# Performance work log

Measured on AMD Instinct MI355X. Metric: run time of the kernel, lower is better.

Reference implementation:

```python
import jax, jax.numpy as jnp
import numpy as np

B, S, H = 2, 2048, 2048
NH, NKV, HD = 16, 4, 128
GROUPS = NH // NKV  # 4
ROPE_BASE = 10000.0


def _rope_tables(seq_len, dim):
    inv_freq = 1.0 / (ROPE_BASE ** (jnp.arange(0, dim, 2, dtype=jnp.float32) / dim))
    t = jnp.arange(seq_len, dtype=jnp.float32)
    freqs = jnp.outer(t, inv_freq)            # [S, HD/2]
    emb = jnp.concatenate([freqs, freqs], -1)  # [S, HD]
    return jnp.cos(emb), jnp.sin(emb)


def _rotate_half(x):
    x1, x2 = x[..., : x.shape[-1] // 2], x[..., x.shape[-1] // 2:]
    return jnp.concatenate([-x2, x1], axis=-1)


def setup_inputs() -> dict:
    key = jax.random.key(0)
    ks = jax.random.split(key, 5)
    hidden_states = jax.random.normal(ks[0], (B, S, H), dtype=jnp.float32)
    wq = jax.random.normal(ks[1], (H, NH * HD), dtype=jnp.float32) * 0.02
    wk = jax.random.normal(ks[2], (H, NKV * HD), dtype=jnp.float32) * 0.02
    wv = jax.random.normal(ks[3], (H, NKV * HD), dtype=jnp.float32) * 0.02
    wo = jax.random.normal(ks[4], (NH * HD, H), dtype=jnp.float32) * 0.02
    # additive causal mask [1,1,S,S]
    causal = jnp.tril(jnp.ones((S, S), dtype=bool))
    attention_mask = jnp.where(causal, 0.0, jnp.finfo(jnp.float32).min)[None, None]
    return {"hidden_states": hidden_states, "attention_mask": attention_mask,
            "wq": wq, "wk": wk, "wv": wv, "wo": wo}


def reference(hidden_states, attention_mask, wq, wk, wv, wo):
    b, s, _ = hidden_states.shape
    # projections -> [B, heads, S, HD]
    q = (hidden_states @ wq).reshape(b, s, NH, HD).transpose(0, 2, 1, 3)
    k = (hidden_states @ wk).reshape(b, s, NKV, HD).transpose(0, 2, 1, 3)
    v = (hidden_states @ wv).reshape(b, s, NKV, HD).transpose(0, 2, 1, 3)
    cos, sin = _rope_tables(s, HD)             # [S, HD]
    cos = cos[None, None]; sin = sin[None, None]
    q = q * cos + _rotate_half(q) * sin
    k = k * cos + _rotate_half(k) * sin
    # GQA: repeat kv heads (matches repeat_interleave on dim=1)
    k = jnp.repeat(k, GROUPS, axis=1)
    v = jnp.repeat(v, GROUPS, axis=1)
    scores = jnp.einsum("bhqd,bhkd->bhqk", q, k) / jnp.sqrt(jnp.float32(HD))
    scores = scores + attention_mask
    probs = jax.nn.softmax(scores.astype(jnp.float32), axis=-1).astype(q.dtype)
    attn = jnp.einsum("bhqk,bhkd->bhqd", probs, v)
    attn = attn.transpose(0, 2, 1, 3).reshape(b, s, NH * HD)
    return attn @ wo
```

## Files before the change

### kernel.cpp

```cpp
#include <hip/hip_runtime.h>

typedef unsigned short u16;
typedef unsigned int u32;
typedef __attribute__((ext_vector_type(8))) __bf16 bf16x8;
typedef __attribute__((ext_vector_type(8))) u16 u16x8;
typedef __attribute__((ext_vector_type(4))) float f32x4;

#define B_ 2
#define S_ 2048
#define H_ 2048
#define NH_ 16
#define NKV_ 4
#define HD_ 128

__device__ __forceinline__ u16 f2bf(float f) {
  return __builtin_bit_cast(u16, static_cast<__bf16>(f));
}
__device__ __forceinline__ float bf2f(u16 v) {
  return __builtin_bit_cast(float, (u32)v << 16);
}
__device__ __forceinline__ void gl2lds16(const void* g, void* l) {
  __builtin_amdgcn_global_load_lds((const __attribute__((address_space(1))) u32*)g,
                                   (__attribute__((address_space(3))) u32*)l, 16, 0, 0);
}
__device__ __forceinline__ f32x4 mfma16(bf16x8 a, bf16x8 b, f32x4 c) {
  return __builtin_amdgcn_mfma_f32_16x16x32_bf16(a, b, c, 0, 0, 0);
}

__global__ __launch_bounds__(256) void cvt_f32_bf16(const float* __restrict__ in,
                                                    u16* __restrict__ out) {
  size_t i = ((size_t)blockIdx.x * 256 + threadIdx.x) * 8;
  const float4* p = (const float4*)(in + i);
  float4 a = p[0], b = p[1];
  u16x8 o;
  o[0] = f2bf(a.x); o[1] = f2bf(a.y); o[2] = f2bf(a.z); o[3] = f2bf(a.w);
  o[4] = f2bf(b.x); o[5] = f2bf(b.y); o[6] = f2bf(b.z); o[7] = f2bf(b.w);
  *(u16x8*)(out + i) = o;
}

__global__ __launch_bounds__(256) void transpose_f32_bf16(const float* __restrict__ in,
                                                          u16* __restrict__ out,
                                                          int R, int C) {
  __shared__ float tl[32][33];
  int bx = blockIdx.x, by = blockIdx.y;
  int tx = threadIdx.x & 31, ty = threadIdx.x >> 5;
#pragma unroll
  for (int i = 0; i < 32; i += 8)
    tl[ty + i][tx] = in[(size_t)(by * 32 + ty + i) * C + bx * 32 + tx];
  __syncthreads();
#pragma unroll
  for (int i = 0; i < 32; i += 8)
    out[(size_t)(bx * 32 + ty + i) * R + by * 32 + tx] = f2bf(tl[tx][ty + i]);
}

__global__ __launch_bounds__(256) void transpose_v(const u16* __restrict__ kvb,
                                                   u16* __restrict__ vt) {
  __shared__ u16 tl[32][33];
  int sx = blockIdx.x, dx = blockIdx.y, b = blockIdx.z;
  int tx = threadIdx.x & 31, ty = threadIdx.x >> 5;
#pragma unroll
  for (int i = 0; i < 32; i += 8)
    tl[ty + i][tx] = kvb[(size_t)(b * S_ + sx * 32 + ty + i) * 1024 + 512 + dx * 32 + tx];
  __syncthreads();
#pragma unroll
  for (int i = 0; i < 32; i += 8)
    vt[(size_t)(b * 512 + dx * 32 + ty + i) * 2048 + sx * 32 + tx] = tl[tx][ty + i];
}

__global__ __launch_bounds__(256) void rope_kernel(u16* __restrict__ buf, int rstride,
                                                   int nhshift, float scale) {
  int idx = blockIdx.x * 256 + threadIdx.x;
  int grp = idx & 7;
  int h = (idx >> 3) & ((1 << nhshift) - 1);
  int tok = idx >> (3 + nhshift);
  int s = tok & (S_ - 1);
  u16* p = buf + (size_t)tok * rstride + (h << 7) + grp * 8;
  u16x8 lo = *(u16x8*)p;
  u16x8 hi = *(u16x8*)(p + 64);
  u16x8 olo, ohi;
#pragma unroll
  for (int j = 0; j < 8; j++) {
    int i = grp * 8 + j;
    float inv = exp2f((float)i * -0.20762050593045702f);
    float ang = (float)s * inv;
    float c = cosf(ang) * scale, sn = sinf(ang) * scale;
    float xl = bf2f(lo[j]), xh = bf2f(hi[j]);
    olo[j] = f2bf(xl * c - xh * sn);
    ohi[j] = f2bf(xh * c + xl * sn);
  }
  *(u16x8*)p = olo;
  *(u16x8*)(p + 64) = ohi;
}

template <int MODE>
__global__ __launch_bounds__(256) void gemm_bt(const u16* __restrict__ A,
                                               const u16* __restrict__ BT,
                                               void* __restrict__ C0,
                                               void* __restrict__ C1,
                                               int M, int N, int K) {
  __shared__ u16 As[2 * 128 * 32];
  __shared__ u16 Bs[2 * 128 * 32];
  const int Mt = M >> 7;
  const int nwg = gridDim.x;
  int wg = (blockIdx.x & 7) * (nwg >> 3) + (blockIdx.x >> 3);
  int tm = wg % Mt, tn = wg / Mt;
  const size_t m0 = (size_t)tm << 7, n0 = (size_t)tn << 7;
  const int tid = threadIdx.x;
  const int w = tid >> 6, lane = tid & 63;
  const int g = lane >> 4, l15 = lane & 15;
  const int wr = w >> 1, wc = w & 1;

  const int r0 = tid >> 2, s0 = tid & 3;
  const int r1 = (tid + 256) >> 2, s1 = (tid + 256) & 3;
  const u16* Ar0 = A + (m0 + r0) * K + s0 * 8;
  const u16* Ar1 = A + (m0 + r1) * K + s1 * 8;
  const u16* Br0 = BT + (n0 + r0) * K + s0 * 8;
  const u16* Br1 = BT + (n0 + r1) * K + s1 * 8;

  const f32x4 Z4 = {0.f, 0.f, 0.f, 0.f};
  f32x4 acc[4][4];
#pragma unroll
  for (int m = 0; m < 4; m++)
#pragma unroll
    for (int n = 0; n < 4; n++) acc[m][n] = Z4;

  gl2lds16(Ar0, &As[w * 512]);
  gl2lds16(Ar1, &As[w * 512 + 2048]);
  gl2lds16(Br0, &Bs[w * 512]);
  gl2lds16(Br1, &Bs[w * 512 + 2048]);

  const int nk = K >> 5;
  int cur = 0;
  for (int t = 0; t < nk; ++t) {
    if (t + 1 < nk) {
      const int k0 = (t + 1) << 5;
      const int nb = (cur ^ 1) << 12;
      gl2lds16(Ar0 + k0, &As[nb + w * 512]);
      gl2lds16(Ar1 + k0, &As[nb + w * 512 + 2048]);
      gl2lds16(Br0 + k0, &Bs[nb + w * 512]);
      gl2lds16(Br1 + k0, &Bs[nb + w * 512 + 2048]);
      asm volatile("s_waitcnt vmcnt(4)" ::: "memory");
    } else {
      asm volatile("s_waitcnt vmcnt(0)" ::: "memory");
    }
    __builtin_amdgcn_sched_barrier(0);
    __builtin_amdgcn_s_barrier();
    __builtin_amdgcn_sched_barrier(0);
    const int cb = cur << 12;
    bf16x8 af[4], bfr[4];
#pragma unroll
    for (int m = 0; m < 4; m++)
      af[m] = *(const bf16x8*)&As[cb + (wr * 64 + m * 16 + l15) * 32 + g * 8];
#pragma unroll
    for (int n = 0; n < 4; n++)
      bfr[n] = *(const bf16x8*)&Bs[cb + (wc * 64 + n * 16 + l15) * 32 + g * 8];
#pragma unroll
    for (int m = 0; m < 4; m++)
#pragma unroll
      for (int n = 0; n < 4; n++) acc[m][n] = mfma16(af[m], bfr[n], acc[m][n]);
    __builtin_amdgcn_sched_barrier(0);
    __builtin_amdgcn_s_barrier();
    __builtin_amdgcn_sched_barrier(0);
    cur ^= 1;
  }

  if (MODE == 2) {
    float* C = (float*)C0;
#pragma unroll
    for (int m = 0; m < 4; m++)
#pragma unroll
      for (int n = 0; n < 4; n++)
#pragma unroll
        for (int r = 0; r < 4; r++) {
          size_t row = m0 + wr * 64 + m * 16 + g * 4 + r;
          size_t col = n0 + wc * 64 + n * 16 + l15;
          C[row * (size_t)N + col] = acc[m][n][r];
        }
  } else {
    u16* C;
    size_t cs, cbase;
    if (n0 < 2048) { C = (u16*)C0; cs = 2048; cbase = n0; }
    else           { C = (u16*)C1; cs = 1024; cbase = n0 - 2048; }
#pragma unroll
    for (int m = 0; m < 4; m++)
#pragma unroll
      for (int n = 0; n < 4; n++)
#pragma unroll
        for (int r = 0; r < 4; r++) {
          size_t row = m0 + wr * 64 + m * 16 + g * 4 + r;
          C[row * cs + cbase + wc * 64 + n * 16 + l15] = f2bf(acc[m][n][r]);
        }
  }
}

__global__ __launch_bounds__(256) void attn_kernel(const u16* __restrict__ Qb,
                                                   const u16* __restrict__ KVb,
                                                   const u16* __restrict__ Vt,
                                                   u16* __restrict__ Ob) {
  __shared__ u16 Ks[2][64 * 128];
  __shared__ u16 Vs[2][128 * 64];
  __shared__ u16 Ps[4][16 * 72];
  const int pair = blockIdx.x, h = blockIdx.y, b = blockIdx.z;
  const int kvh = h >> 2;
  const int tid = threadIdx.x, w = tid >> 6, lane = tid & 63;
  const int g = lane >> 4, l15 = lane & 15;
  const f32x4 Z4 = {0.f, 0.f, 0.f, 0.f};
  u16x8 oneu;
#pragma unroll
  for (int j = 0; j < 8; j++) oneu[j] = 0x3f80;
  const bf16x8 ones = __builtin_bit_cast(bf16x8, oneu);

  const u16* Kbase = KVb + (size_t)b * S_ * 1024 + kvh * 128;
  const u16* Vbase = Vt + (size_t)(b * NKV_ + kvh) * HD_ * 2048;

  for (int half = 0; half < 2; ++half) {
    const int qt = half ? pair : 31 - pair;
    const int qrow0 = qt * 64 + w * 16;

    bf16x8 qf[4];
    const u16* qp = Qb + (size_t)(b * S_ + qrow0 + l15) * 2048 + h * 128;
#pragma unroll
    for (int ds = 0; ds < 4; ds++) qf[ds] = *(const bf16x8*)(qp + ds * 32 + g * 8);

    float m_r[4], l_r[4];
    f32x4 oa[8];
#pragma unroll
    for (int r = 0; r < 4; r++) { m_r[r] = -1e30f; l_r[r] = 0.f; }
#pragma unroll
    for (int n = 0; n < 8; n++) oa[n] = Z4;

    const int nt = qt + 1;
#pragma unroll
    for (int ro = 0; ro < 4; ++ro) {
      int c = ro * 256 + tid;
      int kv = c >> 4, p = c & 15;
      gl2lds16(Kbase + (size_t)kv * 1024 + 8 * (p ^ (kv & 15)), &Ks[0][ro * 2048 + w * 512]);
      int d = c >> 3, p2 = c & 7;
      gl2lds16(Vbase + (size_t)d * 2048 + 8 * (p2 ^ (d & 7)), &Vs[0][ro * 2048 + w * 512]);
    }
    __syncthreads();
    int cur = 0;

    for (int t = 0; t < nt; ++t) {
      const int kv0 = t * 64;
      if (t + 1 < nt) {
        const int nkv0 = kv0 + 64;
#pragma unroll
        for (int ro = 0; ro < 4; ++ro) {
          int c = ro * 256 + tid;
          int kv = c >> 4, p = c & 15;
          gl2lds16(Kbase + (size_t)(nkv0 + kv) * 1024 + 8 * (p ^ (kv & 15)),
                   &Ks[cur ^ 1][ro * 2048 + w * 512]);
          int d = c >> 3, p2 = c & 7;
          gl2lds16(Vbase + (size_t)d * 2048 + nkv0 + 8 * (p2 ^ (d & 7)),
                   &Vs[cur ^ 1][ro * 2048 + w * 512]);
        }
      }

      f32x4 sa[4];
#pragma unroll
      for (int c16 = 0; c16 < 4; c16++) sa[c16] = Z4;
      __builtin_amdgcn_s_setprio(1);
#pragma unroll
      for (int ds = 0; ds < 4; ++ds) {
#pragma unroll
        for (int c16 = 0; c16 < 4; ++c16) {
          bf16x8 kf = *(const bf16x8*)&Ks[cur][(c16 * 16 + l15) * 128 + ((ds * 4 + g) ^ l15) * 8];
          sa[c16] = mfma16(qf[ds], kf, sa[c16]);
        }
      }
      __builtin_amdgcn_s_setprio(0);

      if (kv0 + 63 > qrow0) {
#pragma unroll
        for (int c16 = 0; c16 < 4; c16++)
#pragma unroll
          for (int r = 0; r < 4; r++) {
            if (kv0 + c16 * 16 + l15 > qrow0 + g * 4 + r) sa[c16][r] = -1e30f;
          }
      }

      float lmax[4];
#pragma unroll
      for (int r = 0; r < 4; r++)
        lmax[r] = fmaxf(fmaxf(sa[0][r], sa[1][r]), fmaxf(sa[2][r], sa[3][r]));
      bool need = (lmax[0] > m_r[0] + 11.5415603f) || (lmax[1] > m_r[1] + 11.5415603f) ||
                  (lmax[2] > m_r[2] + 11.5415603f) || (lmax[3] > m_r[3] + 11.5415603f);
      if (__any(need)) {
        float pm[4];
#pragma unroll
        for (int r = 0; r < 4; r++) pm[r] = lmax[r];
#pragma unroll
        for (int off = 1; off < 16; off <<= 1)
#pragma unroll
          for (int r = 0; r < 4; r++) pm[r] = fmaxf(pm[r], __shfl_xor(pm[r], off));
#pragma unroll
        for (int r = 0; r < 4; r++) {
          float mn = fmaxf(m_r[r], pm[r]);
          float corr = exp2f(m_r[r] - mn);
          m_r[r] = mn;
          l_r[r] *= corr;
#pragma unroll
          for (int n = 0; n < 8; n++) oa[n][r] *= corr;
        }
      }

#pragma unroll
      for (int c16 = 0; c16 < 4; c16++)
#pragma unroll
        for (int r = 0; r < 4; r++)
          Ps[w][(g * 4 + r) * 72 + c16 * 16 + l15] =
              f2bf(exp2f(sa[c16][r] - m_r[r]));
      asm volatile("s_waitcnt lgkmcnt(0)" ::: "memory");
      __builtin_amdgcn_sched_barrier(0);

      f32x4 srow = Z4;
      __builtin_amdgcn_s_setprio(1);
#pragma unroll
      for (int ks = 0; ks < 2; ++ks) {
        bf16x8 pa = *(const bf16x8*)&Ps[w][l15 * 72 + ks * 32 + g * 8];
        srow = mfma16(pa, ones, srow);
#pragma unroll
        for (int n = 0; n < 8; n++) {
          bf16x8 vf = *(const bf16x8*)&Vs[cur][(n * 16 + l15) * 64 + (((ks * 4 + g) ^ (l15 & 7))) * 8];
          oa[n] = mfma16(pa, vf, oa[n]);
        }
      }
      __builtin_amdgcn_s_setprio(0);
#pragma unroll
      for (int r = 0; r < 4; r++) l_r[r] += srow[r];

      __syncthreads();
      cur ^= 1;
    }

    float inv[4];
#pragma unroll
    for (int r = 0; r < 4; r++) inv[r] = 1.0f / l_r[r];
#pragma unroll
    for (int n = 0; n < 8; n++)
#pragma unroll
      for (int r = 0; r < 4; r++) {
        size_t row = (size_t)b * S_ + qrow0 + g * 4 + r;
        Ob[row * 2048 + h * 128 + n * 16 + l15] = f2bf(oa[n][r] * inv[r]);
      }
  }
}

extern "C" void kernel_launch(void* const* d_in, const int* in_sizes, int n_in,
                              void* d_out, int out_size, void* d_ws, size_t ws_size,
                              hipStream_t stream) {
  const float* hid = (const float*)d_in[0];
  const float* wq = (const float*)d_in[2];
  const float* wk = (const float*)d_in[3];
  const float* wv = (const float*)d_in[4];
  const float* wo = (const float*)d_in[5];
  float* out = (float*)d_out;
  char* ws = (char*)d_ws;

  u16* hb     = (u16*)(ws);
  u16* wqkvT  = (u16*)(ws + (16u << 20));
  u16* Vt     = (u16*)(ws + (16u << 20));
  u16* woT    = (u16*)(ws + (20u << 20));
  u16* Qb     = (u16*)(ws + (28u << 20));
  u16* KVb    = (u16*)(ws + (44u << 20));

  cvt_f32_bf16<<<4096, 256, 0, stream>>>(hid, hb);
  transpose_f32_bf16<<<dim3(64, 64), 256, 0, stream>>>(wq, wqkvT, 2048, 2048);
  transpose_f32_bf16<<<dim3(16, 64), 256, 0, stream>>>(wk, wqkvT + (size_t)2048 * 2048, 2048, 512);
  transpose_f32_bf16<<<dim3(16, 64), 256, 0, stream>>>(wv, wqkvT + (size_t)2560 * 2048, 2048, 512);

  gemm_bt<1><<<768, 256, 0, stream>>>(hb, wqkvT, Qb, KVb, 4096, 3072, 2048);

  rope_kernel<<<2048, 256, 0, stream>>>(Qb, 2048, 4, 0.1275179064f);
  rope_kernel<<<512, 256, 0, stream>>>(KVb, 1024, 2, 1.0f);

  transpose_v<<<dim3(64, 16, 2), 256, 0, stream>>>(KVb, Vt);
  transpose_f32_bf16<<<dim3(64, 64), 256, 0, stream>>>(wo, woT, 2048, 2048);

  attn_kernel<<<dim3(16, 16, 2), 256, 0, stream>>>(Qb, KVb, Vt, hb);

  gemm_bt<2><<<512, 256, 0, stream>>>(hb, woT, out, nullptr, 4096, 2048, 2048);
}
```

Baseline: 236.6 us.

## Process both paired query tiles in one KV sweep to share K/V loads

The attention kernel previously handled its two paired query tiles (qt and 31-qt) sequentially, streaming K/V tiles twice. Now both tiles' online-softmax states are kept live and each loaded K/V tile is used by both, so the shorter tile's K/V traffic and its separate prologue/sync loop go away. The cost is doubled register state (two sets of Q fragments and output accumulators), which may raise VGPR pressure and lower occupancy. The Ps scratch buffer is also reused back to back for the two tiles within an iteration.

```diff
diff --git a/kernel.cpp b/kernel.cpp
--- a/kernel.cpp
+++ b/kernel.cpp
@@ -193,6 +193,67 @@
   }
 }
 
+#define ATTN_STATE(qf, qrow0, m_r, l_r, oa)                                      \
+  {                                                                              \
+    f32x4 sa[4];                                                                 \
+    _Pragma("unroll") for (int c16 = 0; c16 < 4; c16++) sa[c16] = Z4;            \
+    __builtin_amdgcn_s_setprio(1);                                               \
+    _Pragma("unroll") for (int ds = 0; ds < 4; ++ds) {                           \
+      _Pragma("unroll") for (int c16 = 0; c16 < 4; ++c16) {                      \
+        bf16x8 kf = *(const bf16x8*)&Ks[cur][(c16 * 16 + l15) * 128 +            \
+                                            ((ds * 4 + g) ^ l15) * 8];           \
+        sa[c16] = mfma16(qf[ds], kf, sa[c16]);                                   \
+      }                                                                          \
+    }                                                                            \
+    __builtin_amdgcn_s_setprio(0);                                               \
+    if (kv0 + 63 > (qrow0)) {                                                    \
+      _Pragma("unroll") for (int c16 = 0; c16 < 4; c16++)                        \
+        _Pragma("unroll") for (int r = 0; r < 4; r++) {                          \
+          if (kv0 + c16 * 16 + l15 > (qrow0) + g * 4 + r) sa[c16][r] = -1e30f;   \
+        }                                                                        \
+    }                                                                            \
+    float lmax[4];                                                               \
+    _Pragma("unroll") for (int r = 0; r < 4; r++)                                \
+        lmax[r] = fmaxf(fmaxf(sa[0][r], sa[1][r]), fmaxf(sa[2][r], sa[3][r]));   \
+    bool need = (lmax[0] > m_r[0] + 11.5415603f) ||                              \
+                (lmax[1] > m_r[1] + 11.5415603f) ||                              \
+                (lmax[2] > m_r[2] + 11.5415603f) ||                              \
+                (lmax[3] > m_r[3] + 11.5415603f);                                \
+    if (__any(need)) {                                                           \
+      float pm[4];                                                               \
+      _Pragma("unroll") for (int r = 0; r < 4; r++) pm[r] = lmax[r];             \
+      _Pragma("unroll") for (int off = 1; off < 16; off <<= 1)                   \
+        _Pragma("unroll") for (int r = 0; r < 4; r++)                            \
+            pm[r] = fmaxf(pm[r], __shfl_xor(pm[r], off));                        \
+      _Pragma("unroll") for (int r = 0; r < 4; r++) {                            \
+        float mn = fmaxf(m_r[r], pm[r]);                                         \
+        float corr = exp2f(m_r[r] - mn);                                         \
+        m_r[r] = mn;                                                             \
+        l_r[r] *= corr;                                                          \
+        _Pragma("unroll") for (int n = 0; n < 8; n++) oa[n][r] *= corr;          \
+      }                                                                          \
+    }                                                                            \
+    _Pragma("unroll") for (int c16 = 0; c16 < 4; c16++)                          \
+      _Pragma("unroll") for (int r = 0; r < 4; r++)                              \
+          Ps[w][(g * 4 + r) * 72 + c16 * 16 + l15] =                             \
+              f2bf(exp2f(sa[c16][r] - m_r[r]));                                  \
+    asm volatile("s_waitcnt lgkmcnt(0)" ::: "memory");                           \
+    __builtin_amdgcn_sched_barrier(0);                                           \
+    f32x4 srow = Z4;                                                             \
+    __builtin_amdgcn_s_setprio(1);                                               \
+    _Pragma("unroll") for (int ks = 0; ks < 2; ++ks) {                           \
+      bf16x8 pa = *(const bf16x8*)&Ps[w][l15 * 72 + ks * 32 + g * 8];            \
+      srow = mfma16(pa, ones, srow);                                             \
+      _Pragma("unroll") for (int n = 0; n < 8; n++) {                            \
+        bf16x8 vf = *(const bf16x8*)&Vs[cur][(n * 16 + l15) * 64 +               \
+                                            (((ks * 4 + g) ^ (l15 & 7))) * 8];   \
+        oa[n] = mfma16(pa, vf, oa[n]);                                           \
+      }                                                                          \
+    }                                                                            \
+    __builtin_amdgcn_s_setprio(0);                                               \
+    _Pragma("unroll") for (int r = 0; r < 4; r++) l_r[r] += srow[r];             \
+  }
+
 __global__ __launch_bounds__(256) void attn_kernel(const u16* __restrict__ Qb,
                                                    const u16* __restrict__ KVb,
                                                    const u16* __restrict__ Vt,
@@ -213,138 +274,74 @@
   const u16* Kbase = KVb + (size_t)b * S_ * 1024 + kvh * 128;
   const u16* Vbase = Vt + (size_t)(b * NKV_ + kvh) * HD_ * 2048;
 
-  for (int half = 0; half < 2; ++half) {
-    const int qt = half ? pair : 31 - pair;
-    const int qrow0 = qt * 64 + w * 16;
-
-    bf16x8 qf[4];
-    const u16* qp = Qb + (size_t)(b * S_ + qrow0 + l15) * 2048 + h * 128;
-#pragma unroll
-    for (int ds = 0; ds < 4; ds++) qf[ds] = *(const bf16x8*)(qp + ds * 32 + g * 8);
-
-    float m_r[4], l_r[4];
-    f32x4 oa[8];
-#pragma unroll
-    for (int r = 0; r < 4; r++) { m_r[r] = -1e30f; l_r[r] = 0.f; }
-#pragma unroll
-    for (int n = 0; n < 8; n++) oa[n] = Z4;
-
-    const int nt = qt + 1;
-#pragma unroll
-    for (int ro = 0; ro < 4; ++ro) {
-      int c = ro * 256 + tid;
-      int kv = c >> 4, p = c & 15;
-      gl2lds16(Kbase + (size_t)kv * 1024 + 8 * (p ^ (kv & 15)), &Ks[0][ro * 2048 + w * 512]);
-      int d = c >> 3, p2 = c & 7;
-      gl2lds16(Vbase + (size_t)d * 2048 + 8 * (p2 ^ (d & 7)), &Vs[0][ro * 2048 + w * 512]);
+  const int qtA = 31 - pair, qtB = pair;
+  const int qrowA = qtA * 64 + w * 16, qrowB = qtB * 64 + w * 16;
+
+  bf16x8 qfA[4], qfB[4];
+  {
+    const u16* qpA = Qb + (size_t)(b * S_ + qrowA + l15) * 2048 + h * 128;
+    const u16* qpB = Qb + (size_t)(b * S_ + qrowB + l15) * 2048 + h * 128;
+#pragma unroll
+    for (int ds = 0; ds < 4; ds++) {
+      qfA[ds] = *(const bf16x8*)(qpA + ds * 32 + g * 8);
+      qfB[ds] = *(const bf16x8*)(qpB + ds * 32 + g * 8);
     }
+  }
+
+  float mA[4], lA[4], mB[4], lB[4];
+  f32x4 oaA[8], oaB[8];
+#pragma unroll
+  for (int r = 0; r < 4; r++) { mA[r] = -1e30f; lA[r] = 0.f; mB[r] = -1e30f; lB[r] = 0.f; }
+#pragma unroll
+  for (int n = 0; n < 8; n++) { oaA[n] = Z4; oaB[n] = Z4; }
+
+  const int ntA = qtA + 1, ntB = qtB + 1;
+#pragma unroll
+  for (int ro = 0; ro < 4; ++ro) {
+    int c = ro * 256 + tid;
+    int kv = c >> 4, p = c & 15;
+    gl2lds16(Kbase + (size_t)kv * 1024 + 8 * (p ^ (kv & 15)), &Ks[0][ro * 2048 + w * 512]);
+    int d = c >> 3, p2 = c & 7;
+    gl2lds16(Vbase + (size_t)d * 2048 + 8 * (p2 ^ (d & 7)), &Vs[0][ro * 2048 + w * 512]);
+  }
+  __syncthreads();
+  int cur = 0;
+
+  for (int t = 0; t < ntA; ++t) {
+    const int kv0 = t * 64;
+    if (t + 1 < ntA) {
+      const int nkv0 = kv0 + 64;
+#pragma unroll
+      for (int ro = 0; ro < 4; ++ro) {
+        int c = ro * 256 + tid;
+        int kv = c >> 4, p = c & 15;
+        gl2lds16(Kbase + (size_t)(nkv0 + kv) * 1024 + 8 * (p ^ (kv & 15)),
+                 &Ks[cur ^ 1][ro * 2048 + w * 512]);
+        int d = c >> 3, p2 = c & 7;
+        gl2lds16(Vbase + (size_t)d * 2048 + nkv0 + 8 * (p2 ^ (d & 7)),
+                 &Vs[cur ^ 1][ro * 2048 + w * 512]);
+      }
+    }
+
+    ATTN_STATE(qfA, qrowA, mA, lA, oaA)
+    if (t < ntB) ATTN_STATE(qfB, qrowB, mB, lB, oaB)
+
     __syncthreads();
-    int cur = 0;
-
-    for (int t = 0; t < nt; ++t) {
-      const int kv0 = t * 64;
-      if (t + 1 < nt) {
-        const int nkv0 = kv0 + 64;
-#pragma unroll
-        for (int ro = 0; ro < 4; ++ro) {
-          int c = ro * 256 + tid;
-          int kv = c >> 4, p = c & 15;
-          gl2lds16(Kbase + (size_t)(nkv0 + kv) * 1024 + 8 * (p ^ (kv & 15)),
-                   &Ks[cur ^ 1][ro * 2048 + w * 512]);
-          int d = c >> 3, p2 = c & 7;
-          gl2lds16(Vbase + (size_t)d * 2048 + nkv0 + 8 * (p2 ^ (d & 7)),
-                   &Vs[cur ^ 1][ro * 2048 + w * 512]);
-        }
-      }
-
-      f32x4 sa[4];
-#pragma unroll
-      for (int c16 = 0; c16 < 4; c16++) sa[c16] = Z4;
-      __builtin_amdgcn_s_setprio(1);
-#pragma unroll
-      for (int ds = 0; ds < 4; ++ds) {
-#pragma unroll
-        for (int c16 = 0; c16 < 4; ++c16) {
-          bf16x8 kf = *(const bf16x8*)&Ks[cur][(c16 * 16 + l15) * 128 + ((ds * 4 + g) ^ l15) * 8];
-          sa[c16] = mfma16(qf[ds], kf, sa[c16]);
-        }
-      }
-      __builtin_amdgcn_s_setprio(0);
-
-      if (kv0 + 63 > qrow0) {
-#pragma unroll
-        for (int c16 = 0; c16 < 4; c16++)
-#pragma unroll
-          for (int r = 0; r < 4; r++) {
-            if (kv0 + c16 * 16 + l15 > qrow0 + g * 4 + r) sa[c16][r] = -1e30f;
-          }
-      }
-
-      float lmax[4];
-#pragma unroll
-      for (int r = 0; r < 4; r++)
-        lmax[r] = fmaxf(fmaxf(sa[0][r], sa[1][r]), fmaxf(sa[2][r], sa[3][r]));
-      bool need = (lmax[0] > m_r[0] + 11.5415603f) || (lmax[1] > m_r[1] + 11.5415603f) ||
-                  (lmax[2] > m_r[2] + 11.5415603f) || (lmax[3] > m_r[3] + 11.5415603f);
-      if (__any(need)) {
-        float pm[4];
-#pragma unroll
-        for (int r = 0; r < 4; r++) pm[r] = lmax[r];
-#pragma unroll
-        for (int off = 1; off < 16; off <<= 1)
-#pragma unroll
-          for (int r = 0; r < 4; r++) pm[r] = fmaxf(pm[r], __shfl_xor(pm[r], off));
-#pragma unroll
-        for (int r = 0; r < 4; r++) {
-          float mn = fmaxf(m_r[r], pm[r]);
-          float corr = exp2f(m_r[r] - mn);
-          m_r[r] = mn;
-          l_r[r] *= corr;
-#pragma unroll
-          for (int n = 0; n < 8; n++) oa[n][r] *= corr;
-        }
-      }
-
-#pragma unroll
-      for (int c16 = 0; c16 < 4; c16++)
-#pragma unroll
-        for (int r = 0; r < 4; r++)
-          Ps[w][(g * 4 + r) * 72 + c16 * 16 + l15] =
-              f2bf(exp2f(sa[c16][r] - m_r[r]));
-      asm volatile("s_waitcnt lgkmcnt(0)" ::: "memory");
-      __builtin_amdgcn_sched_barrier(0);
-
-      f32x4 srow = Z4;
-      __builtin_amdgcn_s_setprio(1);
-#pragma unroll
-      for (int ks = 0; ks < 2; ++ks) {
-        bf16x8 pa = *(const bf16x8*)&Ps[w][l15 * 72 + ks * 32 + g * 8];
-        srow = mfma16(pa, ones, srow);
-#pragma unroll
-        for (int n = 0; n < 8; n++) {
-          bf16x8 vf = *(const bf16x8*)&Vs[cur][(n * 16 + l15) * 64 + (((ks * 4 + g) ^ (l15 & 7))) * 8];
-          oa[n] = mfma16(pa, vf, oa[n]);
-        }
-      }
-      __builtin_amdgcn_s_setprio(0);
-#pragma unroll
-      for (int r = 0; r < 4; r++) l_r[r] += srow[r];
-
-      __syncthreads();
-      cur ^= 1;
+    cur ^= 1;
+  }
+
+  float invA[4], invB[4];
+#pragma unroll
+  for (int r = 0; r < 4; r++) { invA[r] = 1.0f / lA[r]; invB[r] = 1.0f / lB[r]; }
+#pragma unroll
+  for (int n = 0; n < 8; n++)
+#pragma unroll
+    for (int r = 0; r < 4; r++) {
+      size_t rowA = (size_t)b * S_ + qrowA + g * 4 + r;
+      size_t rowB = (size_t)b * S_ + qrowB + g * 4 + r;
+      Ob[rowA * 2048 + h * 128 + n * 16 + l15] = f2bf(oaA[n][r] * invA[r]);
+      Ob[rowB * 2048 + h * 128 + n * 16 + l15] = f2bf(oaB[n][r] * invB[r]);
     }
-
-    float inv[4];
-#pragma unroll
-    for (int r = 0; r < 4; r++) inv[r] = 1.0f / l_r[r];
-#pragma unroll
-    for (int n = 0; n < 8; n++)
-#pragma unroll
-      for (int r = 0; r < 4; r++) {
-        size_t row = (size_t)b * S_ + qrow0 + g * 4 + r;
-        Ob[row * 2048 + h * 128 + n * 16 + l15] = f2bf(oa[n][r] * inv[r]);
-      }
-  }
 }
 
 extern "C" void kernel_launch(void* const* d_in, const int* in_sizes, int n_in,
```

New measurement: 289.9 us. 22.5% more time.
